# Kernel tuning notes

Hardware: AMD Instinct MI355X
Metric: run time of the kernel (lower is better)

## Reference

```python
import jax, jax.numpy as jnp
import numpy as np

B, A, D = 512, 32, 256      # batch clips, actors (nodes per graph), feature dim
E = 1048576                 # total edges over the flattened (B*A)-node graph
THRESHOLD = 0.5             # config.knn.threshold
EPS = 1e-5


def setup_inputs() -> dict:
    key = jax.random.key(0)
    k1, k2, k3 = jax.random.split(key, 3)
    N = B * A
    X = jax.random.normal(k1, (B, A, D), dtype=jnp.float32)
    edge_index = jax.random.randint(k2, (2, E), 0, N, dtype=jnp.int32)
    W = jax.random.normal(k3, (D, D), dtype=jnp.float32) * (1.0 / np.sqrt(D))
    b = jnp.zeros((D,), dtype=jnp.float32)
    return {"X": X, "edge_index": edge_index, "W": W, "b": b}


def gcn_conv(x, edge_index, W, b):
    # Standard GCNConv: x' = D^-1/2 (A + I) D^-1/2 (x W) + b
    N = x.shape[0]
    x = x @ W                                            # [N, D]
    loop = jnp.arange(N, dtype=edge_index.dtype)
    src = jnp.concatenate([edge_index[0], loop])         # message sources
    tgt = jnp.concatenate([edge_index[1], loop])         # aggregation targets
    deg = jax.ops.segment_sum(jnp.ones_like(src, dtype=x.dtype), tgt,
                              num_segments=N)            # in-degree incl. self-loop
    dinv = jnp.where(deg > 0, jax.lax.rsqrt(deg), 0.0)
    coef = (dinv[src] * dinv[tgt])[:, None]              # symmetric norm per edge
    out = jax.ops.segment_sum(x[src] * coef, tgt, num_segments=N)
    return out + b


def reference(X, edge_index, W, b):
    Bq, Aq, Dq = X.shape
    x = X.reshape(Bq * Aq, Dq)
    x = gcn_conv(x, edge_index, W, b)
    Xo = x.reshape(Bq, Aq, Dq)

    # cal_edge: pairwise squared distances per batch, min-max normalized,
    # thresholded. Instead of variable-length dense_to_sparse edge lists we
    # return the equivalent fixed-shape adjacency mask [B, A, A].
    inner = -2.0 * jnp.einsum('bad,bcd->bac', Xo, Xo)
    sq = jnp.sum(Xo * Xo, axis=-1, keepdims=True)        # [B, A, 1]
    scores = sq + inner + jnp.swapaxes(sq, -1, -2)       # [B, A, A]
    smin = scores.min(axis=-1, keepdims=True)
    smax = scores.max(axis=-1, keepdims=True)
    scores = (scores - smin) / (smax - smin + EPS)
    adj_mask = scores > THRESHOLD                        # new edge set (dense form)
    return Xo, adj_mask
```

## Files before the change

kernel.cpp:

```cpp
#include <hip/hip_runtime.h>

#define BQ 512
#define AQ 32
#define DQ 256
#define NQ (BQ * AQ)
#define EQ 1048576
#define THR 0.5f
#define EPSF 1e-5f
#define DEG_STRIDE 160
#define BIN_TGTS 64
#define NBINS (NQ / BIN_TGTS)
#define NBLK_P 256
#define EPB (EQ / NBLK_P)

typedef __attribute__((ext_vector_type(8))) short bf16x8;
typedef __attribute__((ext_vector_type(4))) float f32x4;

__device__ __forceinline__ unsigned short f2bf(float f) {
    unsigned int u = __float_as_uint(f);
    return (unsigned short)((u + 0x7FFFu + ((u >> 16) & 1u)) >> 16);
}
__device__ __forceinline__ float bf2f(unsigned short h) {
    return __uint_as_float((unsigned int)h << 16);
}

__global__ __launch_bounds__(256) void k_wt_part(
        const float* __restrict__ W, unsigned short* __restrict__ Wt,
        const int* __restrict__ src, const int* __restrict__ tgt,
        int* __restrict__ cntT, int* __restrict__ offT,
        unsigned int* __restrict__ binned) {
    __shared__ unsigned int buf[EPB];
    __shared__ int hist[NBINS];
    __shared__ int sdat[NBINS];
    __shared__ int cur[NBINS];
    int tid = threadIdx.x;
    if (blockIdx.x < 256) {
        int idx = blockIdx.x * 256 + tid;
        int n = idx >> 8;
        int k = idx & 255;
        float w = W[k * DQ + n];
        unsigned short h = f2bf(w);
        Wt[idx] = h;
        Wt[DQ * DQ + idx] = f2bf(w - bf2f(h));
        return;
    }
    int blk = blockIdx.x - 256;
    hist[tid] = 0;
    __syncthreads();
    int base = blk * EPB;
    int t[16], s[16];
    #pragma unroll
    for (int i = 0; i < 16; i++) {
        int e = base + i * 256 + tid;
        t[i] = tgt[e];
        s[i] = src[e];
        atomicAdd(&hist[t[i] >> 6], 1);
    }
    __syncthreads();
    int v = hist[tid];
    sdat[tid] = v;
    __syncthreads();
    #pragma unroll
    for (int off = 1; off < 256; off <<= 1) {
        int add = (tid >= off) ? sdat[tid - off] : 0;
        __syncthreads();
        sdat[tid] += add;
        __syncthreads();
    }
    int excl = sdat[tid] - v;
    cur[tid] = excl;
    cntT[blk * NBINS + tid] = v;
    offT[blk * NBINS + tid] = excl;
    __syncthreads();
    #pragma unroll
    for (int i = 0; i < 16; i++) {
        int pos = atomicAdd(&cur[t[i] >> 6], 1);
        buf[pos] = ((unsigned int)t[i] << 14) | (unsigned int)s[i];
    }
    __syncthreads();
    unsigned int* g = binned + (size_t)blk * EPB;
    #pragma unroll
    for (int i = 0; i < 16; i++) g[i * 256 + tid] = buf[i * 256 + tid];
}

__global__ __launch_bounds__(256) void k_gemm_bucket(
        const float* __restrict__ Xp, const unsigned short* __restrict__ Wt,
        unsigned short* __restrict__ xwb,
        const int* __restrict__ cntT, const int* __restrict__ offT,
        const unsigned int* __restrict__ binned,
        unsigned short* __restrict__ bucket, int* __restrict__ cnt,
        float* __restrict__ dinv) {
    __shared__ unsigned short bs[2][256 * 40];
    __shared__ int lcnt[BIN_TGTS];
    int tid = threadIdx.x;
    if (blockIdx.x >= 256) {
        unsigned short* lbuck = &bs[0][0];
        int b = blockIdx.x - 256;
        if (tid < BIN_TGTS) lcnt[tid] = 0;
        __syncthreads();
        int c = cntT[tid * NBINS + b];
        int o = offT[tid * NBINS + b];
        const unsigned int* e = binned + (size_t)tid * EPB + o;
        for (int j = 0; j < c; j++) {
            unsigned int ed = e[j];
            int tl = (int)(ed >> 14) & 63;
            int pos = atomicAdd(&lcnt[tl], 1);
            if (pos < DEG_STRIDE)
                lbuck[tl * DEG_STRIDE + pos] = (unsigned short)(ed & 0x3FFFu);
        }
        __syncthreads();
        const unsigned int* lb32 = (const unsigned int*)lbuck;
        unsigned int* gb32 = (unsigned int*)(bucket + (size_t)b * BIN_TGTS * DEG_STRIDE);
        #pragma unroll
        for (int i = 0; i < 20; i++) gb32[i * 256 + tid] = lb32[i * 256 + tid];
        if (tid < BIN_TGTS) {
            int cc = lcnt[tid];
            cnt[b * BIN_TGTS + tid] = cc;
            dinv[b * BIN_TGTS + tid] = rsqrtf((float)(cc + 1));
        }
        return;
    }
    int wave = tid >> 6;
    int lane = tid & 63;
    int col = lane & 15;
    int quad = lane >> 4;
    int mbase = blockIdx.x * 64 + wave * 16;
    int m = mbase + col;

    const float* arow = Xp + (size_t)m * DQ;
    const unsigned short* Wlo = Wt + DQ * DQ;

    f32x4 acc[16];
    f32x4 zero = {0.f, 0.f, 0.f, 0.f};
    #pragma unroll
    for (int i = 0; i < 16; i++) acc[i] = zero;

    for (int k0 = 0; k0 < DQ; k0 += 32) {
        __syncthreads();
        {
            const uint4* gh = (const uint4*)(Wt + tid * DQ + k0);
            const uint4* gl = (const uint4*)(Wlo + tid * DQ + k0);
            uint4* lh = (uint4*)&bs[0][tid * 40];
            uint4* ll = (uint4*)&bs[1][tid * 40];
            #pragma unroll
            for (int u = 0; u < 4; u++) lh[u] = gh[u];
            #pragma unroll
            for (int u = 0; u < 4; u++) ll[u] = gl[u];
        }
        __syncthreads();

        int kq = k0 + quad * 8;
        float4 a0 = *(const float4*)(arow + kq);
        float4 a1 = *(const float4*)(arow + kq + 4);
        float av[8] = {a0.x, a0.y, a0.z, a0.w, a1.x, a1.y, a1.z, a1.w};
        bf16x8 ah, al;
        #pragma unroll
        for (int j = 0; j < 8; j++) {
            unsigned short h = f2bf(av[j]);
            ah[j] = (short)h;
            al[j] = (short)f2bf(av[j] - bf2f(h));
        }
        #pragma unroll
        for (int nt = 0; nt < 16; nt++) {
            int n = nt * 16 + col;
            bf16x8 bh = *(const bf16x8*)&bs[0][n * 40 + quad * 8];
            bf16x8 bl = *(const bf16x8*)&bs[1][n * 40 + quad * 8];
            acc[nt] = __builtin_amdgcn_mfma_f32_16x16x32_bf16(ah, bh, acc[nt], 0, 0, 0);
            acc[nt] = __builtin_amdgcn_mfma_f32_16x16x32_bf16(al, bh, acc[nt], 0, 0, 0);
            acc[nt] = __builtin_amdgcn_mfma_f32_16x16x32_bf16(ah, bl, acc[nt], 0, 0, 0);
        }
    }

    #pragma unroll
    for (int nt = 0; nt < 16; nt++) {
        #pragma unroll
        for (int r = 0; r < 4; r++) {
            xwb[(size_t)(mbase + quad * 4 + r) * DQ + nt * 16 + col] =
                f2bf(acc[nt][r]);
        }
    }
}

__global__ __launch_bounds__(512) void k_agg_scores(
        const unsigned int* __restrict__ xwb,
        const int* __restrict__ cnt,
        const unsigned short* __restrict__ bucket,
        const float* __restrict__ dinv,
        const float* __restrict__ bias,
        float* __restrict__ out,
        float* __restrict__ mask) {
    __shared__ float xs[AQ][DQ + 4];
    __shared__ float sq[AQ];
    __shared__ float sc[AQ][AQ + 1];
    __shared__ float rmin[AQ], rmax[AQ];

    int tid = threadIdx.x;
    int wave = tid >> 6;
    int lane = tid & 63;
    int bq = blockIdx.x;
    const uint2* xw2 = (const uint2*)xwb;

    float4 bv = ((const float4*)bias)[lane];

    #pragma unroll 1
    for (int i = 0; i < 4; i++) {
        int a = wave * 4 + i;
        int t = bq * AQ + a;
        float dt = dinv[t];
        float c0 = dt * dt;
        uint2 sp = xw2[(size_t)t * 64 + lane];
        float4 acc;
        acc.x = __uint_as_float(sp.x << 16) * c0;
        acc.y = __uint_as_float(sp.x & 0xFFFF0000u) * c0;
        acc.z = __uint_as_float(sp.y << 16) * c0;
        acc.w = __uint_as_float(sp.y & 0xFFFF0000u) * c0;

        const unsigned short* brow = bucket + (size_t)t * DEG_STRIDE;
        int num = cnt[t];
        if (num > DEG_STRIDE) num = DEG_STRIDE;
        for (int k0 = 0; k0 < num; k0 += 64) {
            int rem = num - k0;
            int n = rem < 64 ? rem : 64;
            int idx = k0 + (lane < n ? lane : 0);
            int e = (int)brow[idx];
            float cl = (lane < n) ? dinv[e] * dt : 0.f;
            int n8 = (n + 7) & ~7;
            for (int j0 = 0; j0 < n8; j0 += 8) {
                #pragma unroll
                for (int jj = 0; jj < 8; jj++) {
                    int j = j0 + jj;
                    int s = __shfl(e, j);
                    float c = __shfl(cl, j);
                    uint2 p = xw2[(size_t)s * 64 + lane];
                    acc.x += __uint_as_float(p.x << 16) * c;
                    acc.y += __uint_as_float(p.x & 0xFFFF0000u) * c;
                    acc.z += __uint_as_float(p.y << 16) * c;
                    acc.w += __uint_as_float(p.y & 0xFFFF0000u) * c;
                }
            }
        }

        acc.x += bv.x; acc.y += bv.y; acc.z += bv.z; acc.w += bv.w;
        ((float4*)out)[(size_t)t * 64 + lane] = acc;
        *(float4*)&xs[a][lane * 4] = acc;
    }
    __syncthreads();

    if (tid < AQ) {
        const float4* xi = (const float4*)xs[tid];
        float s = 0.f;
        #pragma unroll 8
        for (int dd = 0; dd < DQ / 4; dd++) {
            float4 a = xi[dd];
            s += a.x * a.x + a.y * a.y + a.z * a.z + a.w * a.w;
        }
        sq[tid] = s;
    }
    __syncthreads();

    {
        int p0 = tid * 2;
        int i = p0 >> 5;
        int j0 = p0 & 31;
        const float4* xi = (const float4*)xs[i];
        float g[2] = {0.f, 0.f};
        for (int dd = 0; dd < DQ / 4; dd += 8) {
            float4 ar[8];
            #pragma unroll
            for (int u = 0; u < 8; u++) ar[u] = xi[dd + u];
            #pragma unroll
            for (int q = 0; q < 2; q++) {
                const float4* xj = (const float4*)xs[j0 + q];
                float gq = 0.f;
                #pragma unroll
                for (int u = 0; u < 8; u++) {
                    float4 b = xj[dd + u];
                    gq += ar[u].x * b.x + ar[u].y * b.y +
                          ar[u].z * b.z + ar[u].w * b.w;
                }
                g[q] += gq;
            }
        }
        #pragma unroll
        for (int q = 0; q < 2; q++) {
            sc[i][j0 + q] = sq[i] - 2.f * g[q] + sq[j0 + q];
        }
    }
    __syncthreads();

    if (tid < AQ) {
        float mn = sc[tid][0], mx = sc[tid][0];
        for (int j = 1; j < AQ; j++) {
            float v = sc[tid][j];
            mn = fminf(mn, v);
            mx = fmaxf(mx, v);
        }
        rmin[tid] = mn;
        rmax[tid] = mx;
    }
    __syncthreads();

    {
        float* mb = mask + (size_t)bq * AQ * AQ;
        int p0 = tid * 2;
        int i = p0 >> 5, j0 = p0 & 31;
        float inv = 1.0f / (rmax[i] - rmin[i] + EPSF);
        float2 mv;
        mv.x = ((sc[i][j0 + 0] - rmin[i]) * inv > THR) ? 1.0f : 0.0f;
        mv.y = ((sc[i][j0 + 1] - rmin[i]) * inv > THR) ? 1.0f : 0.0f;
        ((float2*)mb)[tid] = mv;
    }
}

extern "C" void kernel_launch(void* const* d_in, const int* in_sizes, int n_in,
                              void* d_out, int out_size, void* d_ws, size_t ws_size,
                              hipStream_t stream) {
    const float* X    = (const float*)d_in[0];
    const int*   ei   = (const int*)d_in[1];
    const float* W    = (const float*)d_in[2];
    const float* bias = (const float*)d_in[3];
    float* out = (float*)d_out;

    char* ws = (char*)d_ws;
    unsigned short* xwb = (unsigned short*)ws;
    unsigned int* binned = (unsigned int*)(ws + (size_t)NQ * DQ * 2);
    unsigned short* bucket = (unsigned short*)(binned + (size_t)NBLK_P * EPB);
    unsigned short* Wt = bucket + (size_t)NQ * DEG_STRIDE;
    float* dinv = (float*)(Wt + 2 * DQ * DQ);
    int* cnt = (int*)(dinv + NQ);
    int* cntT = cnt + NQ;
    int* offT = cntT + NBLK_P * NBINS;

    const int* src = ei;
    const int* tgt = ei + EQ;

    k_wt_part<<<512, 256, 0, stream>>>(W, Wt, src, tgt, cntT, offT, binned);
    k_gemm_bucket<<<512, 256, 0, stream>>>(X, Wt, xwb, cntT, offT, binned,
                                           bucket, cnt, dinv);
    k_agg_scores<<<BQ, 512, 0, stream>>>((const unsigned int*)xwb, cnt, bucket,
                                         dinv, bias, out,
                                         out + (size_t)NQ * DQ);
}
```

Baseline: 163.6 us.

## Fuse edge partition with GEMM and split W bf16 conversion into GEMM loads

Removes the separate W transpose/bf16 split pass by having each GEMM block read fp32 W directly and convert it to hi/lo bf16 while staging into shared memory. The edge partition now runs alongside the GEMM in one launch, and bucketing moves to its own kernel. The goal is to drop the Wt intermediate and rebalance work so the GEMM no longer waits behind the transpose. The cost is that every GEMM block repeats the W conversion, and the W loads are strided scalar reads instead of vector loads.

Result: slower. 168.0 us (+2.7%).

```diff
diff --git a/kernel.cpp b/kernel.cpp
--- a/kernel.cpp
+++ b/kernel.cpp
@@ -24,111 +24,66 @@
     return __uint_as_float((unsigned int)h << 16);
 }
 
-__global__ __launch_bounds__(256) void k_wt_part(
-        const float* __restrict__ W, unsigned short* __restrict__ Wt,
+__global__ __launch_bounds__(256) void k_part_gemm(
+        const float* __restrict__ W, const float* __restrict__ Xp,
+        unsigned short* __restrict__ xwb,
         const int* __restrict__ src, const int* __restrict__ tgt,
         int* __restrict__ cntT, int* __restrict__ offT,
         unsigned int* __restrict__ binned) {
-    __shared__ unsigned int buf[EPB];
-    __shared__ int hist[NBINS];
-    __shared__ int sdat[NBINS];
-    __shared__ int cur[NBINS];
+    __shared__ unsigned short bs[2][256 * 40];
     int tid = threadIdx.x;
     if (blockIdx.x < 256) {
-        int idx = blockIdx.x * 256 + tid;
-        int n = idx >> 8;
-        int k = idx & 255;
-        float w = W[k * DQ + n];
-        unsigned short h = f2bf(w);
-        Wt[idx] = h;
-        Wt[DQ * DQ + idx] = f2bf(w - bf2f(h));
-        return;
-    }
-    int blk = blockIdx.x - 256;
-    hist[tid] = 0;
-    __syncthreads();
-    int base = blk * EPB;
-    int t[16], s[16];
-    #pragma unroll
-    for (int i = 0; i < 16; i++) {
-        int e = base + i * 256 + tid;
-        t[i] = tgt[e];
-        s[i] = src[e];
-        atomicAdd(&hist[t[i] >> 6], 1);
-    }
-    __syncthreads();
-    int v = hist[tid];
-    sdat[tid] = v;
-    __syncthreads();
-    #pragma unroll
-    for (int off = 1; off < 256; off <<= 1) {
-        int add = (tid >= off) ? sdat[tid - off] : 0;
-        __syncthreads();
-        sdat[tid] += add;
-        __syncthreads();
-    }
-    int excl = sdat[tid] - v;
-    cur[tid] = excl;
-    cntT[blk * NBINS + tid] = v;
-    offT[blk * NBINS + tid] = excl;
-    __syncthreads();
-    #pragma unroll
-    for (int i = 0; i < 16; i++) {
-        int pos = atomicAdd(&cur[t[i] >> 6], 1);
-        buf[pos] = ((unsigned int)t[i] << 14) | (unsigned int)s[i];
-    }
-    __syncthreads();
-    unsigned int* g = binned + (size_t)blk * EPB;
-    #pragma unroll
-    for (int i = 0; i < 16; i++) g[i * 256 + tid] = buf[i * 256 + tid];
-}
-
-__global__ __launch_bounds__(256) void k_gemm_bucket(
-        const float* __restrict__ Xp, const unsigned short* __restrict__ Wt,
-        unsigned short* __restrict__ xwb,
-        const int* __restrict__ cntT, const int* __restrict__ offT,
-        const unsigned int* __restrict__ binned,
-        unsigned short* __restrict__ bucket, int* __restrict__ cnt,
-        float* __restrict__ dinv) {
-    __shared__ unsigned short bs[2][256 * 40];
-    __shared__ int lcnt[BIN_TGTS];
-    int tid = threadIdx.x;
-    if (blockIdx.x >= 256) {
-        unsigned short* lbuck = &bs[0][0];
-        int b = blockIdx.x - 256;
-        if (tid < BIN_TGTS) lcnt[tid] = 0;
-        __syncthreads();
-        int c = cntT[tid * NBINS + b];
-        int o = offT[tid * NBINS + b];
-        const unsigned int* e = binned + (size_t)tid * EPB + o;
-        for (int j = 0; j < c; j++) {
-            unsigned int ed = e[j];
-            int tl = (int)(ed >> 14) & 63;
-            int pos = atomicAdd(&lcnt[tl], 1);
-            if (pos < DEG_STRIDE)
-                lbuck[tl * DEG_STRIDE + pos] = (unsigned short)(ed & 0x3FFFu);
-        }
-        __syncthreads();
-        const unsigned int* lb32 = (const unsigned int*)lbuck;
-        unsigned int* gb32 = (unsigned int*)(bucket + (size_t)b * BIN_TGTS * DEG_STRIDE);
-        #pragma unroll
-        for (int i = 0; i < 20; i++) gb32[i * 256 + tid] = lb32[i * 256 + tid];
-        if (tid < BIN_TGTS) {
-            int cc = lcnt[tid];
-            cnt[b * BIN_TGTS + tid] = cc;
-            dinv[b * BIN_TGTS + tid] = rsqrtf((float)(cc + 1));
-        }
+        unsigned int* buf = (unsigned int*)&bs[0][0];
+        int* hist = (int*)((char*)bs + 16 * 1024);
+        int* sdat = hist + NBINS;
+        int* cur  = sdat + NBINS;
+        int blk = blockIdx.x;
+        hist[tid] = 0;
+        __syncthreads();
+        int base = blk * EPB;
+        int t[16], s[16];
+        #pragma unroll
+        for (int i = 0; i < 16; i++) {
+            int e = base + i * 256 + tid;
+            t[i] = tgt[e];
+            s[i] = src[e];
+            atomicAdd(&hist[t[i] >> 6], 1);
+        }
+        __syncthreads();
+        int v = hist[tid];
+        sdat[tid] = v;
+        __syncthreads();
+        #pragma unroll
+        for (int off = 1; off < 256; off <<= 1) {
+            int add = (tid >= off) ? sdat[tid - off] : 0;
+            __syncthreads();
+            sdat[tid] += add;
+            __syncthreads();
+        }
+        int excl = sdat[tid] - v;
+        cur[tid] = excl;
+        cntT[blk * NBINS + tid] = v;
+        offT[blk * NBINS + tid] = excl;
+        __syncthreads();
+        #pragma unroll
+        for (int i = 0; i < 16; i++) {
+            int pos = atomicAdd(&cur[t[i] >> 6], 1);
+            buf[pos] = ((unsigned int)t[i] << 14) | (unsigned int)s[i];
+        }
+        __syncthreads();
+        unsigned int* g = binned + (size_t)blk * EPB;
+        #pragma unroll
+        for (int i = 0; i < 16; i++) g[i * 256 + tid] = buf[i * 256 + tid];
         return;
     }
     int wave = tid >> 6;
     int lane = tid & 63;
     int col = lane & 15;
     int quad = lane >> 4;
-    int mbase = blockIdx.x * 64 + wave * 16;
+    int mbase = (blockIdx.x - 256) * 64 + wave * 16;
     int m = mbase + col;
 
     const float* arow = Xp + (size_t)m * DQ;
-    const unsigned short* Wlo = Wt + DQ * DQ;
 
     f32x4 acc[16];
     f32x4 zero = {0.f, 0.f, 0.f, 0.f};
@@ -138,14 +93,22 @@
     for (int k0 = 0; k0 < DQ; k0 += 32) {
         __syncthreads();
         {
-            const uint4* gh = (const uint4*)(Wt + tid * DQ + k0);
-            const uint4* gl = (const uint4*)(Wlo + tid * DQ + k0);
-            uint4* lh = (uint4*)&bs[0][tid * 40];
-            uint4* ll = (uint4*)&bs[1][tid * 40];
+            unsigned int hw[16], lw[16];
             #pragma unroll
-            for (int u = 0; u < 4; u++) lh[u] = gh[u];
+            for (int p = 0; p < 16; p++) {
+                float w0 = W[(size_t)(k0 + 2 * p) * DQ + tid];
+                float w1 = W[(size_t)(k0 + 2 * p + 1) * DQ + tid];
+                unsigned short h0 = f2bf(w0);
+                unsigned short h1 = f2bf(w1);
+                hw[p] = (unsigned int)h0 | ((unsigned int)h1 << 16);
+                unsigned short l0 = f2bf(w0 - bf2f(h0));
+                unsigned short l1 = f2bf(w1 - bf2f(h1));
+                lw[p] = (unsigned int)l0 | ((unsigned int)l1 << 16);
+            }
+            unsigned int* lh = (unsigned int*)&bs[0][tid * 40];
+            unsigned int* ll = (unsigned int*)&bs[1][tid * 40];
             #pragma unroll
-            for (int u = 0; u < 4; u++) ll[u] = gl[u];
+            for (int u = 0; u < 16; u++) { lh[u] = hw[u]; ll[u] = lw[u]; }
         }
         __syncthreads();
 
@@ -178,6 +141,39 @@
             xwb[(size_t)(mbase + quad * 4 + r) * DQ + nt * 16 + col] =
                 f2bf(acc[nt][r]);
         }
+    }
+}
+
+__global__ __launch_bounds__(256) void k_bucket(
+        const int* __restrict__ cntT, const int* __restrict__ offT,
+        const unsigned int* __restrict__ binned,
+        unsigned short* __restrict__ bucket, int* __restrict__ cnt,
+        float* __restrict__ dinv) {
+    __shared__ unsigned short lbuck[BIN_TGTS * DEG_STRIDE];
+    __shared__ int lcnt[BIN_TGTS];
+    int tid = threadIdx.x;
+    int b = blockIdx.x;
+    if (tid < BIN_TGTS) lcnt[tid] = 0;
+    __syncthreads();
+    int c = cntT[tid * NBINS + b];
+    int o = offT[tid * NBINS + b];
+    const unsigned int* e = binned + (size_t)tid * EPB + o;
+    for (int j = 0; j < c; j++) {
+        unsigned int ed = e[j];
+        int tl = (int)(ed >> 14) & 63;
+        int pos = atomicAdd(&lcnt[tl], 1);
+        if (pos < DEG_STRIDE)
+            lbuck[tl * DEG_STRIDE + pos] = (unsigned short)(ed & 0x3FFFu);
+    }
+    __syncthreads();
+    const unsigned int* lb32 = (const unsigned int*)lbuck;
+    unsigned int* gb32 = (unsigned int*)(bucket + (size_t)b * BIN_TGTS * DEG_STRIDE);
+    #pragma unroll
+    for (int i = 0; i < 20; i++) gb32[i * 256 + tid] = lb32[i * 256 + tid];
+    if (tid < BIN_TGTS) {
+        int cc = lcnt[tid];
+        cnt[b * BIN_TGTS + tid] = cc;
+        dinv[b * BIN_TGTS + tid] = rsqrtf((float)(cc + 1));
     }
 }
 
@@ -325,8 +321,7 @@
     unsigned short* xwb = (unsigned short*)ws;
     unsigned int* binned = (unsigned int*)(ws + (size_t)NQ * DQ * 2);
     unsigned short* bucket = (unsigned short*)(binned + (size_t)NBLK_P * EPB);
-    unsigned short* Wt = bucket + (size_t)NQ * DEG_STRIDE;
-    float* dinv = (float*)(Wt + 2 * DQ * DQ);
+    float* dinv = (float*)(bucket + (size_t)NQ * DEG_STRIDE);
     int* cnt = (int*)(dinv + NQ);
     int* cntT = cnt + NQ;
     int* offT = cntT + NBLK_P * NBINS;
@@ -334,9 +329,8 @@
     const int* src = ei;
     const int* tgt = ei + EQ;
 
-    k_wt_part<<<512, 256, 0, stream>>>(W, Wt, src, tgt, cntT, offT, binned);
-    k_gemm_bucket<<<512, 256, 0, stream>>>(X, Wt, xwb, cntT, offT, binned,
-                                           bucket, cnt, dinv);
+    k_part_gemm<<<512, 256, 0, stream>>>(W, X, xwb, src, tgt, cntT, offT, binned);
+    k_bucket<<<NBINS, 256, 0, stream>>>(cntT, offT, binned, bucket, cnt, dinv);
     k_agg_scores<<<BQ, 512, 0, stream>>>((const unsigned int*)xwb, cnt, bucket,
                                          dinv, bias, out,
                                          out + (size_t)NQ * DQ);
```
